# Performance work log

Measured on AMD Instinct MI355X. Metric: run time of the kernel, lower is better.

## Reference

```python
import jax, jax.numpy as jnp
import numpy as np

C = 16          # image channels (scaled from 1 for production-scale traffic)
GX = 36         # CORTIAL_WIDTH_COUNT
GY = 36         # CORTIAL_HEIGHT_COUNT
RF = 24         # receptive field size
IMG = 64        # image H = W
GAMMA_E = 0.9
GAMMA_I = 0.9


def setup_inputs() -> dict:
    key = jax.random.key(0)
    ks = jax.random.split(key, 7)
    x = jax.random.normal(ks[0], (C, IMG, IMG), dtype=jnp.float32)
    prev_activity = jax.random.uniform(ks[1], (C, GX, GY), dtype=jnp.float32)
    afferent_weights = jax.random.normal(ks[2], (C, GX, GY, RF, RF), dtype=jnp.float32) * 0.05
    ex_lateral_weights = jax.random.normal(ks[3], (C, GX, GY, GX, GY), dtype=jnp.float32) * 0.05
    in_lateral_weights = jax.random.normal(ks[4], (C, GX, GY, GX, GY), dtype=jnp.float32) * 0.05
    rx = jnp.sort(jax.random.randint(ks[5], (GX,), 0, IMG - RF + 1, dtype=jnp.int32))
    ry = jnp.sort(jax.random.randint(ks[6], (GY,), 0, IMG - RF + 1, dtype=jnp.int32))
    return {
        "x": x,
        "prev_activity": prev_activity,
        "afferent_weights": afferent_weights,
        "ex_lateral_weights": ex_lateral_weights,
        "in_lateral_weights": in_lateral_weights,
        "rx": rx,
        "ry": ry,
    }


def reference(x, prev_activity, afferent_weights, ex_lateral_weights, in_lateral_weights, rx, ry):
    # Gather all receptive-field patches at once: patches[c,i,j,u,v] = x[c, rx[i]+u, ry[j]+v]
    u = jnp.arange(RF)
    ix = (rx[:, None] + u)[:, None, :, None]   # [GX,1,RF,1]
    iy = (ry[:, None] + u)[None, :, None, :]   # [1,GY,1,RF]
    patches = x[:, ix, iy]                     # [C,GX,GY,RF,RF]

    # afferent_activation[:,i,j] = sum(patch * W_a[:,i,j]) (scalar broadcast across channels)
    aff = jnp.einsum('cijuv,cijuv->ij', patches, afferent_weights)
    # lateral activations: sum(prev[:,i,j] * W[:,i,j]) over all elements
    exc = jnp.einsum('cij,cijxy->ij', prev_activity, ex_lateral_weights)
    inh = jnp.einsum('cij,cijxy->ij', prev_activity, in_lateral_weights)

    total = aff + GAMMA_E * exc - GAMMA_I * inh   # [GX,GY]
    activity = jnp.maximum(total, 0.0)            # clamp(min=0) sigmoid approximation
    return jnp.broadcast_to(activity[None, :, :], (C, GX, GY))
```

## Files before the change

### kernel.cpp

```cpp
#include <hip/hip_runtime.h>


constexpr int C   = 16;
constexpr int GX  = 36;
constexpr int GY  = 36;
constexpr int RF  = 24;
constexpr int IMG = 64;
constexpr int GG  = GX * GY;
constexpr int RR  = RF * RF;

__global__ __launch_bounds__(256)
void cortex_kernel(const float* __restrict__ x,
                   const float* __restrict__ prev,
                   const float* __restrict__ affW,
                   const float* __restrict__ exW,
                   const float* __restrict__ inW,
                   const int*   __restrict__ rx,
                   const int*   __restrict__ ry,
                   float* __restrict__ out)
{
    const int bid = blockIdx.x;
    const int i = bid / GY;
    const int j = bid - i * GY;
    const int t = threadIdx.x;

    const int rxi = rx[i];
    const int ryj = ry[j];

    float acc = 0.0f;

    {
        const size_t ij = (size_t)bid;
        for (int k = t; k < C * RR; k += 256) {
            const int c = k / RR;
            const int r = k - c * RR;
            const int u = r / RF;
            const int v = r - u * RF;
            const float w  = affW[((size_t)c * GG + ij) * RR + r];
            const float px = x[(c * IMG + rxi + u) * IMG + ryj + v];
            acc = fmaf(w, px, acc);
        }
    }

    {
        float lat = 0.0f;
        for (int c = 0; c < C; ++c) {
            const float p = prev[c * GG + bid];
            const size_t base = ((size_t)c * GG + bid) * GG;
            const float4* e4 = (const float4*)(exW + base);
            const float4* i4 = (const float4*)(inW + base);
            float s = 0.0f;
            for (int k = t; k < GG / 4; k += 256) {
                const float4 a = e4[k];
                const float4 b = i4[k];
                s += (a.x + a.y + a.z + a.w) - (b.x + b.y + b.z + b.w);
            }
            lat = fmaf(p, s, lat);
        }
        acc = fmaf(0.9f, lat, acc);
    }

    for (int off = 32; off > 0; off >>= 1)
        acc += __shfl_down(acc, off, 64);

    __shared__ float sred[4];
    __shared__ float s_act;
    const int wave = t >> 6;
    const int lane = t & 63;
    if (lane == 0) sred[wave] = acc;
    __syncthreads();
    if (t == 0) {
        const float tot = sred[0] + sred[1] + sred[2] + sred[3];
        s_act = fmaxf(tot, 0.0f);
    }
    __syncthreads();

    if (t < C)
        out[t * GG + bid] = s_act;
}

extern "C" void kernel_launch(void* const* d_in, const int* in_sizes, int n_in,
                              void* d_out, int out_size, void* d_ws, size_t ws_size,
                              hipStream_t stream) {
    const float* x     = (const float*)d_in[0];
    const float* prev  = (const float*)d_in[1];
    const float* affW  = (const float*)d_in[2];
    const float* exW   = (const float*)d_in[3];
    const float* inW   = (const float*)d_in[4];
    const int*   rx    = (const int*)d_in[5];
    const int*   ry    = (const int*)d_in[6];
    float* out = (float*)d_out;

    cortex_kernel<<<GG, 256, 0, stream>>>(x, prev, affW, exW, inW, rx, ry, out);
}
```

Before: 285.2 us.

## Split channel work across four blocks per cell and reduce in second kernel

The work for each cortical cell is split over four blocks, each handling four channels, so the grid grows from 1296 to 5184 blocks. Partial sums go to a workspace and a second kernel adds them, applies ReLU and broadcasts to the output. The afferent loop is vectorised with float4 weight loads, and the lateral loop issues loads for several channels at once to raise memory-level parallelism. The cost is an extra kernel launch and a workspace round trip. The lateral loop still leaves threads idle, since only 324 float4s are spread over 256 threads.

```diff
diff --git a/kernel.cpp b/kernel.cpp
--- a/kernel.cpp
+++ b/kernel.cpp
@@ -8,20 +8,25 @@
 constexpr int IMG = 64;
 constexpr int GG  = GX * GY;
 constexpr int RR  = RF * RF;
+constexpr int SPLIT = 4;
+constexpr int CPB   = C / SPLIT;
 
 __global__ __launch_bounds__(256)
-void cortex_kernel(const float* __restrict__ x,
+void cortex_phase1(const float* __restrict__ x,
                    const float* __restrict__ prev,
                    const float* __restrict__ affW,
                    const float* __restrict__ exW,
                    const float* __restrict__ inW,
                    const int*   __restrict__ rx,
                    const int*   __restrict__ ry,
-                   float* __restrict__ out)
+                   float* __restrict__ partial)
 {
-    const int bid = blockIdx.x;
-    const int i = bid / GY;
-    const int j = bid - i * GY;
+    const int bid   = blockIdx.x;
+    const int ij    = bid % GG;
+    const int split = bid / GG;
+    const int cs    = split * CPB;
+    const int i = ij / GY;
+    const int j = ij - i * GY;
     const int t = threadIdx.x;
 
     const int rxi = rx[i];
@@ -29,34 +34,45 @@
 
     float acc = 0.0f;
 
-    {
-        const size_t ij = (size_t)bid;
-        for (int k = t; k < C * RR; k += 256) {
-            const int c = k / RR;
-            const int r = k - c * RR;
-            const int u = r / RF;
-            const int v = r - u * RF;
-            const float w  = affW[((size_t)c * GG + ij) * RR + r];
-            const float px = x[(c * IMG + rxi + u) * IMG + ryj + v];
-            acc = fmaf(w, px, acc);
+    if (t < RR / 4) {
+        const int u  = t / (RF / 4);
+        const int v0 = 4 * (t - u * (RF / 4));
+        float4 w[CPB];
+        #pragma unroll
+        for (int cc = 0; cc < CPB; ++cc) {
+            const int c = cs + cc;
+            w[cc] = ((const float4*)(affW + ((size_t)c * GG + ij) * RR))[t];
+        }
+        #pragma unroll
+        for (int cc = 0; cc < CPB; ++cc) {
+            const int c = cs + cc;
+            const float* xp = x + ((c * IMG + rxi + u) * IMG + ryj + v0);
+            acc = fmaf(w[cc].x, xp[0], acc);
+            acc = fmaf(w[cc].y, xp[1], acc);
+            acc = fmaf(w[cc].z, xp[2], acc);
+            acc = fmaf(w[cc].w, xp[3], acc);
         }
     }
 
+    float d[CPB] = {0.0f, 0.0f, 0.0f, 0.0f};
+    for (int k = t; k < GG / 4; k += 256) {
+        float4 e[CPB], h[CPB];
+        #pragma unroll
+        for (int cc = 0; cc < CPB; ++cc) {
+            const size_t base = ((size_t)(cs + cc) * GG + ij) * GG;
+            e[cc] = ((const float4*)(exW + base))[k];
+            h[cc] = ((const float4*)(inW + base))[k];
+        }
+        #pragma unroll
+        for (int cc = 0; cc < CPB; ++cc)
+            d[cc] += (e[cc].x + e[cc].y + e[cc].z + e[cc].w)
+                   - (h[cc].x + h[cc].y + h[cc].z + h[cc].w);
+    }
     {
         float lat = 0.0f;
-        for (int c = 0; c < C; ++c) {
-            const float p = prev[c * GG + bid];
-            const size_t base = ((size_t)c * GG + bid) * GG;
-            const float4* e4 = (const float4*)(exW + base);
-            const float4* i4 = (const float4*)(inW + base);
-            float s = 0.0f;
-            for (int k = t; k < GG / 4; k += 256) {
-                const float4 a = e4[k];
-                const float4 b = i4[k];
-                s += (a.x + a.y + a.z + a.w) - (b.x + b.y + b.z + b.w);
-            }
-            lat = fmaf(p, s, lat);
-        }
+        #pragma unroll
+        for (int cc = 0; cc < CPB; ++cc)
+            lat = fmaf(prev[(cs + cc) * GG + ij], d[cc], lat);
         acc = fmaf(0.9f, lat, acc);
     }
 
@@ -64,19 +80,26 @@
         acc += __shfl_down(acc, off, 64);
 
     __shared__ float sred[4];
-    __shared__ float s_act;
     const int wave = t >> 6;
     const int lane = t & 63;
     if (lane == 0) sred[wave] = acc;
     __syncthreads();
-    if (t == 0) {
-        const float tot = sred[0] + sred[1] + sred[2] + sred[3];
-        s_act = fmaxf(tot, 0.0f);
+    if (t == 0)
+        partial[split * GG + ij] = sred[0] + sred[1] + sred[2] + sred[3];
+}
+
+__global__ __launch_bounds__(256)
+void cortex_phase2(const float* __restrict__ partial, float* __restrict__ out)
+{
+    const int ij = blockIdx.x * blockDim.x + threadIdx.x;
+    if (ij < GG) {
+        const float tot = partial[ij] + partial[GG + ij]
+                        + partial[2 * GG + ij] + partial[3 * GG + ij];
+        const float a = fmaxf(tot, 0.0f);
+        #pragma unroll
+        for (int c = 0; c < C; ++c)
+            out[c * GG + ij] = a;
     }
-    __syncthreads();
-
-    if (t < C)
-        out[t * GG + bid] = s_act;
 }
 
 extern "C" void kernel_launch(void* const* d_in, const int* in_sizes, int n_in,
@@ -89,7 +112,9 @@
     const float* inW   = (const float*)d_in[4];
     const int*   rx    = (const int*)d_in[5];
     const int*   ry    = (const int*)d_in[6];
-    float* out = (float*)d_out;
+    float* out     = (float*)d_out;
+    float* partial = (float*)d_ws;
 
-    cortex_kernel<<<GG, 256, 0, stream>>>(x, prev, affW, exW, inW, rx, ry, out);
+    cortex_phase1<<<GG * SPLIT, 256, 0, stream>>>(x, prev, affW, exW, inW, rx, ry, partial);
+    cortex_phase2<<<(GG + 255) / 256, 256, 0, stream>>>(partial, out);
 }
```

Result: faster. 273.3 us (-4.2%).

## Widen blocks to 1024 threads and issue all weight loads up front, nontemporal

Applied to the files above, without the earlier changes.

Raises the block size to 1024 threads and fully unrolls the work per thread. Each thread issues its afferent float4 loads, and each wave issues a full lateral weight row, up front rather than in serial loops. Weight loads use nontemporal hints to avoid polluting the cache with streamed data. This increases memory-level parallelism for the bandwidth-bound ~200MB weight stream, at the cost of higher register pressure and fewer resident blocks per CU.

```diff
diff --git a/kernel.cpp b/kernel.cpp
--- a/kernel.cpp
+++ b/kernel.cpp
@@ -9,20 +9,24 @@
 constexpr int GG  = GX * GY;
 constexpr int RR  = RF * RF;
 
-__global__ __launch_bounds__(256)
-void cortex_kernel(const float* __restrict__ x,
-                   const float* __restrict__ prev,
-                   const float* __restrict__ affW,
-                   const float* __restrict__ exW,
-                   const float* __restrict__ inW,
-                   const int*   __restrict__ rx,
-                   const int*   __restrict__ ry,
-                   float* __restrict__ out)
+typedef float f4 __attribute__((ext_vector_type(4)));
+
+__global__ __launch_bounds__(1024)
+void cortex_fused(const float* __restrict__ x,
+                  const float* __restrict__ prev,
+                  const float* __restrict__ affW,
+                  const float* __restrict__ exW,
+                  const float* __restrict__ inW,
+                  const int*   __restrict__ rx,
+                  const int*   __restrict__ ry,
+                  float* __restrict__ out)
 {
-    const int bid = blockIdx.x;
-    const int i = bid / GY;
-    const int j = bid - i * GY;
-    const int t = threadIdx.x;
+    const int ij = blockIdx.x;
+    const int i = ij / GY;
+    const int j = ij - i * GY;
+    const unsigned t    = threadIdx.x;
+    const unsigned wave = t >> 6;
+    const unsigned lane = t & 63u;
 
     const int rxi = rx[i];
     const int ryj = ry[j];
@@ -30,53 +34,83 @@
     float acc = 0.0f;
 
     {
-        const size_t ij = (size_t)bid;
-        for (int k = t; k < C * RR; k += 256) {
-            const int c = k / RR;
-            const int r = k - c * RR;
-            const int u = r / RF;
-            const int v = r - u * RF;
-            const float w  = affW[((size_t)c * GG + ij) * RR + r];
-            const float px = x[(c * IMG + rxi + u) * IMG + ryj + v];
-            acc = fmaf(w, px, acc);
+        constexpr unsigned NAF = C * RR / 4;
+        const unsigned k0 = t;
+        const unsigned k1 = t + 1024u;
+        const bool has2   = t < (NAF - 2048u);
+        const unsigned k2 = has2 ? (t + 2048u) : 0u;
+
+        const unsigned cl0 = k0 / 144u, co0 = k0 - cl0 * 144u;
+        const unsigned cl1 = k1 / 144u, co1 = k1 - cl1 * 144u;
+        const unsigned cl2 = k2 / 144u, co2 = k2 - cl2 * 144u;
+
+        const f4 w0 = __builtin_nontemporal_load(
+            (const f4*)(affW + ((size_t)cl0 * GG + ij) * RR) + co0);
+        const f4 w1 = __builtin_nontemporal_load(
+            (const f4*)(affW + ((size_t)cl1 * GG + ij) * RR) + co1);
+        f4 w2 = (f4)(0.0f);
+        if (has2)
+            w2 = __builtin_nontemporal_load(
+                (const f4*)(affW + ((size_t)cl2 * GG + ij) * RR) + co2);
+
+        const unsigned u0 = co0 / 6u, v0 = (co0 - u0 * 6u) * 4u;
+        const unsigned u1 = co1 / 6u, v1 = (co1 - u1 * 6u) * 4u;
+        const unsigned u2 = co2 / 6u, v2 = (co2 - u2 * 6u) * 4u;
+
+        const float* xp0 = x + ((cl0 * IMG + rxi + u0) * IMG + ryj + v0);
+        const float* xp1 = x + ((cl1 * IMG + rxi + u1) * IMG + ryj + v1);
+        const float* xp2 = x + ((cl2 * IMG + rxi + u2) * IMG + ryj + v2);
+
+        acc = fmaf(w0.x, xp0[0], acc); acc = fmaf(w0.y, xp0[1], acc);
+        acc = fmaf(w0.z, xp0[2], acc); acc = fmaf(w0.w, xp0[3], acc);
+        acc = fmaf(w1.x, xp1[0], acc); acc = fmaf(w1.y, xp1[1], acc);
+        acc = fmaf(w1.z, xp1[2], acc); acc = fmaf(w1.w, xp1[3], acc);
+        if (has2) {
+            acc = fmaf(w2.x, xp2[0], acc); acc = fmaf(w2.y, xp2[1], acc);
+            acc = fmaf(w2.z, xp2[2], acc); acc = fmaf(w2.w, xp2[3], acc);
         }
     }
 
-    {
-        float lat = 0.0f;
-        for (int c = 0; c < C; ++c) {
-            const float p = prev[c * GG + bid];
-            const size_t base = ((size_t)c * GG + bid) * GG;
-            const float4* e4 = (const float4*)(exW + base);
-            const float4* i4 = (const float4*)(inW + base);
-            float s = 0.0f;
-            for (int k = t; k < GG / 4; k += 256) {
-                const float4 a = e4[k];
-                const float4 b = i4[k];
-                s += (a.x + a.y + a.z + a.w) - (b.x + b.y + b.z + b.w);
-            }
-            lat = fmaf(p, s, lat);
-        }
-        acc = fmaf(0.9f, lat, acc);
+    #pragma unroll
+    for (int rr = 0; rr < 2; ++rr) {
+        const int r = (int)wave + rr * 16;
+        const int c = r >> 1;
+        const float* tb = (r & 1) ? inW : exW;
+        const f4* row = (const f4*)(tb + ((size_t)c * GG + ij) * (size_t)GG);
+        const float coeff = prev[c * GG + ij] * ((r & 1) ? -0.9f : 0.9f);
+
+        f4 v[6];
+        #pragma unroll
+        for (int m = 0; m < 5; ++m)
+            v[m] = __builtin_nontemporal_load(row + lane + m * 64u);
+        v[5] = (f4)(0.0f);
+        if (lane < 4u)
+            v[5] = __builtin_nontemporal_load(row + 320u + lane);
+
+        float s = 0.0f;
+        #pragma unroll
+        for (int m = 0; m < 6; ++m)
+            s += (v[m].x + v[m].y) + (v[m].z + v[m].w);
+        acc = fmaf(coeff, s, acc);
     }
 
     for (int off = 32; off > 0; off >>= 1)
         acc += __shfl_down(acc, off, 64);
 
-    __shared__ float sred[4];
+    __shared__ float sred[16];
     __shared__ float s_act;
-    const int wave = t >> 6;
-    const int lane = t & 63;
     if (lane == 0) sred[wave] = acc;
     __syncthreads();
     if (t == 0) {
-        const float tot = sred[0] + sred[1] + sred[2] + sred[3];
+        float tot = 0.0f;
+        #pragma unroll
+        for (int w = 0; w < 16; ++w) tot += sred[w];
         s_act = fmaxf(tot, 0.0f);
     }
     __syncthreads();
 
     if (t < C)
-        out[t * GG + bid] = s_act;
+        out[t * GG + ij] = s_act;
 }
 
 extern "C" void kernel_launch(void* const* d_in, const int* in_sizes, int n_in,
@@ -91,5 +125,5 @@
     const int*   ry    = (const int*)d_in[6];
     float* out = (float*)d_out;
 
-    cortex_kernel<<<GG, 256, 0, stream>>>(x, prev, affW, exW, inW, rx, ry, out);
+    cortex_fused<<<GG, 1024, 0, stream>>>(x, prev, affW, exW, inW, rx, ry, out);
 }
```

After: 247.0 us. -13.4%, faster.
